# Performance work log

Hardware: AMD Instinct MI355X
Metric: run time of the kernel (lower is better)

## Reference

```python
import jax, jax.numpy as jnp
import numpy as np

ALPHA = 0.2
NEG = -9e15
LAYER_OUT = 2


def gat_layer(h, adj, W, a, concat):
    # h: (b,n,in), W: (in,out), a: (2*out,)
    # Faithful to GATLayer: e[i,j] = leaky_relu(a1.Wh_i + a2.Wh_j), computed
    # without materializing the (b,N,N,2F) repeat_interleave tensor.
    Wh = h @ W                               # (b,n,F)
    F = Wh.shape[-1]
    src = jnp.einsum('bnf,f->bn', Wh, a[:F])  # a1 . Wh_i
    dst = jnp.einsum('bnf,f->bn', Wh, a[F:])  # a2 . Wh_j
    e = jax.nn.leaky_relu(src[:, :, None] + dst[:, None, :], ALPHA)  # (b,n,n)
    att = jax.nn.softmax(jnp.where(adj > 0, e, NEG), axis=-1)
    hp = jnp.einsum('bij,bjf->bif', att, Wh)  # bmm aggregation
    return jax.nn.elu(hp) if concat else hp


def setup_inputs() -> dict:
    key = jax.random.key(0)
    ks = jax.random.split(key, 16)
    b, N, L = 16, 512, 1024
    comp_dim, prot_dim, gat_dim, H, latent = 128, 128, 64, 4, 128
    num_atom, num_amino, layer_cnn, window = 100, 30, 3, 5
    k = 2 * window + 1
    s = 0.1
    inp = {
        'atoms': jax.random.randint(ks[0], (b, N), 0, num_atom),
        'atoms_mask': jnp.ones((b, N), jnp.float32),
        'adjacency': jax.random.randint(ks[1], (b, N, N), 0, 2).astype(jnp.int32),
        'amino': jax.random.randint(ks[2], (b, L), 0, num_amino),
        'amino_mask': jnp.ones((b, L), jnp.float32),
        'E_atom': jax.random.normal(ks[3], (num_atom, comp_dim)) * s,
        'E_amino': jax.random.normal(ks[4], (num_amino, prot_dim)) * s,
        'W_gat': jax.random.normal(ks[5], (H, comp_dim, gat_dim)) * s,
        'a_gat': jax.random.normal(ks[6], (H, 2 * gat_dim)) * s,
        'W_go': jax.random.normal(ks[7], (gat_dim * H, comp_dim)) * s,
        'a_go': jax.random.normal(ks[8], (2 * comp_dim,)) * s,
        'W_comp_w': jax.random.normal(ks[9], (latent, comp_dim)) * s,
        'W_comp_b': jnp.zeros((latent,), jnp.float32),
        'conv_w': jax.random.normal(ks[10], (layer_cnn, 1, 1, k, k)) * s,
        'conv_b': jnp.zeros((layer_cnn, 1), jnp.float32),
        'W_att_w': jax.random.normal(ks[11], (latent, latent)) * s,
        'W_att_b': jnp.zeros((latent,), jnp.float32),
        'pred_w': jax.random.normal(ks[12], (1, 2 * latent)) * s,
        'pred_b': jnp.zeros((1,), jnp.float32),
    }
    return inp


def reference(atoms, atoms_mask, adjacency, amino, amino_mask,
              E_atom, E_amino, W_gat, a_gat, W_go, a_go,
              W_comp_w, W_comp_b, conv_w, conv_b,
              W_att_w, W_att_b, pred_w, pred_b):
    # ---- comp_gat (eval mode: dropout is identity) ----
    av = E_atom[atoms]                                      # (b,N,comp_dim)
    H = W_gat.shape[0]
    heads = [gat_layer(av, adjacency, W_gat[i], a_gat[i], True) for i in range(H)]
    multi = jnp.concatenate(heads, axis=-1)                 # (b,N,H*gat_dim)
    x = jax.nn.elu(gat_layer(multi, adjacency, W_go, a_go, False))
    atoms_vec = jax.nn.leaky_relu(x @ W_comp_w.T + W_comp_b, ALPHA)  # (b,N,latent)
    # ---- prot_cnn ----
    pv = E_amino[amino][:, None, :, :]                      # (b,1,L,prot_dim)
    for i in range(conv_w.shape[0]):
        pv = jax.nn.relu(
            jax.lax.conv_general_dilated(
                pv, conv_w[i], (1, 1), 'SAME',
                dimension_numbers=('NCHW', 'OIHW', 'NCHW'))
            + conv_b[i][None, :, None, None])
    amino_vec = pv[:, 0]                                    # (b,L,prot_dim)
    # ---- bidirectional_attention_prediction ----
    a_v = jax.nn.leaky_relu(atoms_vec @ W_att_w.T + W_att_b, ALPHA)
    p_v = jax.nn.leaky_relu(amino_vec @ W_att_w.T + W_att_b, ALPHA)
    prot = (p_v * amino_mask[:, :, None]).sum(1) / amino_mask.sum(1, keepdims=True)
    comp = (a_v * atoms_mask[:, :, None]).sum(1) / atoms_mask.sum(1, keepdims=True)
    cp = jnp.concatenate([comp, prot], axis=1)              # (b,2*latent)
    for _ in range(LAYER_OUT):
        cp = jax.nn.leaky_relu(cp, ALPHA)
    return cp @ pred_w.T + pred_b                           # (b,1)
```

## Files before the change

### kernel.cpp

```cpp
#include <hip/hip_runtime.h>
#include <hip/hip_bf16.h>

typedef __hip_bfloat16 bf16;

#define ALPHA 0.2f
#define NEGV  -9.0e15f
#define TI 8

__device__ __forceinline__ float b2f(bf16 x){ return __bfloat162float(x); }
__device__ __forceinline__ bf16  f2b(float x){ return __float2bfloat16(x); }
__device__ __forceinline__ float lrelu(float x){ return x > 0.f ? x : ALPHA*x; }
__device__ __forceinline__ float eluf(float x){ return x > 0.f ? x : expm1f(x); }

#define P_ATOMS_MASK 0
#define P_AMINO_MASK 8192
#define P_E_ATOM     24576
#define P_E_AMINO    37376
#define P_W_GAT      41216
#define P_A_GAT      73984
#define P_W_GO       74496
#define P_A_GO       107264
#define P_W_COMP_W   107520
#define P_W_COMP_B   123904
#define P_CONV_W     124032
#define P_CONV_B     124395
#define P_W_ATT_W    124398
#define P_W_ATT_B    140782
#define P_PRED_W     140910
#define P_PRED_B     141166
#define P_TOTAL      141167

__device__ __forceinline__ int detect_f32(const unsigned short* u, int n)
{
    int lim = n < 64 ? n : 64;
    bool f32like = false;
    for (int i = 0; i < lim; i += 2) {
        unsigned short h = u[i];
        int e = (h >> 7) & 0xFF;
        bool z = (h & 0x7FFF) == 0;
        if (!(z || (e >= 0x66 && e <= 0x88))) f32like = true;
    }
    if (!f32like && lim > 1 && (u[0] & 0x7FFF) == 0 && (u[1] & 0x7FFF) != 0)
        f32like = true;
    return f32like ? 1 : 0;
}
__device__ __forceinline__ float cvt_elem(const void* src, int e, int mode)
{
    return mode ? ((const float*)src)[e] : b2f(((const bf16*)src)[e]);
}

__global__ __launch_bounds__(256) void k_prep_a(
    const void* p0, const void* p1, const void* p2, const void* p3,
    const void* p4, const void* p5, const void* p6, const void* p7,
    float* __restrict__ params)
{
    const void* ps[8] = {p0,p1,p2,p3,p4,p5,p6,p7};
    const int offs[9] = {0,8192,24576,37376,41216,73984,74496,107264,107520};
    int idx = blockIdx.x*256 + threadIdx.x;
    if (idx >= 107520) return;
    int k = 0;
    while (idx >= offs[k+1]) ++k;
    int mode = detect_f32((const unsigned short*)ps[k], offs[k+1]-offs[k]);
    params[idx] = cvt_elem(ps[k], idx - offs[k], mode);
}

__global__ __launch_bounds__(256) void k_prep_b(
    const void* p0, const void* p1, const void* p2, const void* p3,
    const void* p4, const void* p5, const void* p6, const void* p7,
    float* __restrict__ params)
{
    const void* ps[8] = {p0,p1,p2,p3,p4,p5,p6,p7};
    const int offs[9] = {107520,123904,124032,124395,124398,140782,140910,141166,P_TOTAL};
    int idx = blockIdx.x*256 + threadIdx.x + 107520;
    if (idx >= P_TOTAL) return;
    int k = 0;
    while (idx >= offs[k+1]) ++k;
    int mode = detect_f32((const unsigned short*)ps[k], offs[k+1]-offs[k]);
    params[idx] = cvt_elem(ps[k], idx - offs[k], mode);
}

__global__ __launch_bounds__(256) void k_gat1_pre(
    const int* __restrict__ atoms, const float* __restrict__ params,
    bf16* __restrict__ Wh1, float* __restrict__ src1, float* __restrict__ dst1)
{
    int bid = blockIdx.x;
    int b = bid >> 9, n = bid & 511;
    int tid = threadIdx.x;
    __shared__ float av[128];
    if (tid < 128) av[tid] = params[P_E_ATOM + atoms[bid]*128 + tid];
    __syncthreads();
    int h = tid >> 6, f = tid & 63;
    const float* Wp = params + P_W_GAT + h*8192 + f;
    float wh = 0.f;
    #pragma unroll 8
    for (int k = 0; k < 128; ++k) wh += av[k] * Wp[k*64];
    Wh1[(size_t)bid*256 + h*64 + f] = f2b(wh);
    float p1 = wh * params[P_A_GAT + h*128 + f];
    float p2 = wh * params[P_A_GAT + h*128 + 64 + f];
    #pragma unroll
    for (int m = 32; m; m >>= 1) { p1 += __shfl_xor(p1, m, 64); p2 += __shfl_xor(p2, m, 64); }
    if (f == 0) { src1[(b*4+h)*512 + n] = p1; dst1[(b*4+h)*512 + n] = p2; }
}

__global__ __launch_bounds__(256) void k_gat1_att_b(
    const int* __restrict__ adj, const bf16* __restrict__ Wh1,
    const float* __restrict__ src1, const float* __restrict__ dst1,
    bf16* __restrict__ multi)
{
    int bid = blockIdx.x;
    int b = bid >> 6, i0 = (bid & 63) * TI;
    int tid = threadIdx.x;
    int h = tid >> 6, lane = tid & 63;
    __shared__ float att[4][TI][512];
    const float* dstp = dst1 + (b*4+h)*512;
    float invr[TI];
    #pragma unroll
    for (int ti = 0; ti < TI; ++ti) {
        int i = i0 + ti;
        const int* adjrow = adj + ((size_t)(b*512 + i))*512;
        float s_i = src1[(b*4+h)*512 + i];
        float e[8];
        float lm = -3.0e38f;
        #pragma unroll
        for (int jj = 0; jj < 8; ++jj) {
            int j = lane + jj*64;
            float v = lrelu(s_i + dstp[j]);
            v = adjrow[j] > 0 ? v : NEGV;
            e[jj] = v;
            lm = fmaxf(lm, v);
        }
        #pragma unroll
        for (int m = 32; m; m >>= 1) lm = fmaxf(lm, __shfl_xor(lm, m, 64));
        float ls = 0.f;
        #pragma unroll
        for (int jj = 0; jj < 8; ++jj) {
            float ex = __expf(e[jj] - lm);
            att[h][ti][lane + jj*64] = ex;
            ls += ex;
        }
        #pragma unroll
        for (int m = 32; m; m >>= 1) ls += __shfl_xor(ls, m, 64);
        invr[ti] = 1.f / ls;
    }
    const bf16* Whp = Wh1 + (size_t)(b*512)*256 + h*64 + lane;
    float acc[TI];
    #pragma unroll
    for (int ti = 0; ti < TI; ++ti) acc[ti] = 0.f;
    for (int j = 0; j < 512; ++j) {
        float w = b2f(Whp[(size_t)j*256]);
        #pragma unroll
        for (int ti = 0; ti < TI; ++ti)
            acc[ti] += att[h][ti][j] * w;
    }
    #pragma unroll
    for (int ti = 0; ti < TI; ++ti) {
        float hp = acc[ti] * invr[ti];
        multi[(size_t)(b*512 + i0 + ti)*256 + h*64 + lane] = f2b(eluf(hp));
    }
}

__global__ __launch_bounds__(128) void k_gat2_pre(
    const bf16* __restrict__ multi, const float* __restrict__ params,
    bf16* __restrict__ Wh2, float* __restrict__ src2, float* __restrict__ dst2)
{
    int bid = blockIdx.x;
    int tid = threadIdx.x;
    __shared__ float row[256];
    __shared__ float sr[2][2];
    row[tid]       = b2f(multi[(size_t)bid*256 + tid]);
    row[tid + 128] = b2f(multi[(size_t)bid*256 + tid + 128]);
    __syncthreads();
    const float* Wp = params + P_W_GO;
    float wh = 0.f;
    #pragma unroll 8
    for (int k = 0; k < 256; ++k) wh += row[k] * Wp[k*128 + tid];
    Wh2[(size_t)bid*128 + tid] = f2b(wh);
    float p1 = wh * params[P_A_GO + tid];
    float p2 = wh * params[P_A_GO + 128 + tid];
    #pragma unroll
    for (int m = 32; m; m >>= 1) { p1 += __shfl_xor(p1, m, 64); p2 += __shfl_xor(p2, m, 64); }
    int wid = tid >> 6;
    if ((tid & 63) == 0) { sr[0][wid] = p1; sr[1][wid] = p2; }
    __syncthreads();
    if (tid == 0) src2[bid] = sr[0][0] + sr[0][1];
    if (tid == 1) dst2[bid] = sr[1][0] + sr[1][1];
}

__global__ __launch_bounds__(256) void k_gat2_att_b(
    const int* __restrict__ adj, const bf16* __restrict__ Wh2,
    const float* __restrict__ src2, const float* __restrict__ dst2,
    bf16* __restrict__ x)
{
    int bid = blockIdx.x;
    int b = bid >> 6, i0 = (bid & 63) * TI;
    int tid = threadIdx.x;
    int wv = tid >> 6, lane = tid & 63;
    __shared__ float att[TI][512];
    __shared__ float red[TI][256];
    __shared__ float invs[TI];
    const float* dstp = dst2 + b*512;
    for (int ti = wv; ti < TI; ti += 4) {
        int i = i0 + ti;
        const int* adjrow = adj + ((size_t)(b*512 + i))*512;
        float s_i = src2[b*512 + i];
        float e[8];
        float lm = -3.0e38f;
        #pragma unroll
        for (int jj = 0; jj < 8; ++jj) {
            int j = lane + jj*64;
            float v = lrelu(s_i + dstp[j]);
            v = adjrow[j] > 0 ? v : NEGV;
            e[jj] = v;
            lm = fmaxf(lm, v);
        }
        #pragma unroll
        for (int m = 32; m; m >>= 1) lm = fmaxf(lm, __shfl_xor(lm, m, 64));
        float ls = 0.f;
        #pragma unroll
        for (int jj = 0; jj < 8; ++jj) {
            float ex = __expf(e[jj] - lm);
            att[ti][lane + jj*64] = ex;
            ls += ex;
        }
        #pragma unroll
        for (int m = 32; m; m >>= 1) ls += __shfl_xor(ls, m, 64);
        if (lane == 0) invs[ti] = 1.f / ls;
    }
    __syncthreads();
    int f = tid & 127, c = tid >> 7;
    const bf16* Whp = Wh2 + (size_t)(b*512)*128 + f;
    float acc[TI];
    #pragma unroll
    for (int ti = 0; ti < TI; ++ti) acc[ti] = 0.f;
    int j0 = c * 256;
    for (int j = j0; j < j0 + 256; ++j) {
        float w = b2f(Whp[(size_t)j*128]);
        #pragma unroll
        for (int ti = 0; ti < TI; ++ti)
            acc[ti] += att[ti][j] * w;
    }
    #pragma unroll
    for (int ti = 0; ti < TI; ++ti) red[ti][tid] = acc[ti];
    __syncthreads();
    if (c == 0) {
        #pragma unroll
        for (int ti = 0; ti < TI; ++ti) {
            float hp = (red[ti][f] + red[ti][f+128]) * invs[ti];
            x[(size_t)(b*512 + i0 + ti)*128 + f] = f2b(eluf(hp));
        }
    }
}

#define RM_ROWS 32
__global__ __launch_bounds__(256) void k_rowmat_tile(
    const bf16* __restrict__ in, const float* __restrict__ W,
    const float* __restrict__ bias, bf16* __restrict__ outv)
{
    __shared__ float wlds[128*129];
    __shared__ float rlds[RM_ROWS][128];
    int tid = threadIdx.x;
    size_t row0 = (size_t)blockIdx.x * RM_ROWS;
    for (int idx = tid; idx < 16384; idx += 256)
        wlds[(idx >> 7)*129 + (idx & 127)] = W[idx];
    for (int idx = tid; idx < RM_ROWS*128; idx += 256)
        rlds[idx >> 7][idx & 127] = b2f(in[row0*128 + idx]);
    __syncthreads();
    int l = tid & 127, g = tid >> 7;
    float bl = bias[l];
    #pragma unroll
    for (int rg = 0; rg < 16; rg += 4) {
        int r0 = 2*rg + g;
        float a0=0.f, a1=0.f, a2=0.f, a3=0.f;
        for (int k = 0; k < 128; ++k) {
            float w = wlds[l*129 + k];
            a0 += rlds[r0][k]*w;   a1 += rlds[r0+2][k]*w;
            a2 += rlds[r0+4][k]*w; a3 += rlds[r0+6][k]*w;
        }
        outv[(row0 + r0  )*128 + l] = f2b(lrelu(a0+bl));
        outv[(row0 + r0+2)*128 + l] = f2b(lrelu(a1+bl));
        outv[(row0 + r0+4)*128 + l] = f2b(lrelu(a2+bl));
        outv[(row0 + r0+6)*128 + l] = f2b(lrelu(a3+bl));
    }
}

__global__ __launch_bounds__(256) void k_att_acc_tile(
    const bf16* __restrict__ in, const float* __restrict__ W,
    const float* __restrict__ bias, const float* __restrict__ mask,
    float* __restrict__ acc, int per_b)
{
    __shared__ float wlds[128*129];
    __shared__ float rlds[RM_ROWS][128];
    __shared__ float mlds[RM_ROWS];
    __shared__ float psum[128];
    int tid = threadIdx.x;
    size_t row0 = (size_t)blockIdx.x * RM_ROWS;
    int b = (int)(row0 / per_b);
    for (int idx = tid; idx < 16384; idx += 256)
        wlds[(idx >> 7)*129 + (idx & 127)] = W[idx];
    for (int idx = tid; idx < RM_ROWS*128; idx += 256)
        rlds[idx >> 7][idx & 127] = b2f(in[row0*128 + idx]);
    if (tid < RM_ROWS) mlds[tid] = mask[row0 + tid];
    __syncthreads();
    int l = tid & 127, g = tid >> 7;
    float bl = bias[l];
    float vsum = 0.f;
    #pragma unroll
    for (int rg = 0; rg < 16; rg += 4) {
        int r0 = 2*rg + g;
        float a0=0.f, a1=0.f, a2=0.f, a3=0.f;
        for (int k = 0; k < 128; ++k) {
            float w = wlds[l*129 + k];
            a0 += rlds[r0][k]*w;   a1 += rlds[r0+2][k]*w;
            a2 += rlds[r0+4][k]*w; a3 += rlds[r0+6][k]*w;
        }
        vsum += lrelu(a0+bl)*mlds[r0]   + lrelu(a1+bl)*mlds[r0+2]
              + lrelu(a2+bl)*mlds[r0+4] + lrelu(a3+bl)*mlds[r0+6];
    }
    if (g == 1) psum[l] = vsum;
    __syncthreads();
    if (g == 0) atomicAdd(&acc[b*128 + l], vsum + psum[l]);
}

__global__ __launch_bounds__(128) void k_conv(
    const bf16* __restrict__ in, const int* __restrict__ amino,
    const float* __restrict__ params, bf16* __restrict__ out,
    int layer, int first)
{
    int bid = blockIdx.x;
    int b = bid >> 10, i = bid & 1023;
    int tid = threadIdx.x;
    __shared__ float tile[11][139];
    __shared__ float wts[121];
    __shared__ float bias;
    if (tid < 121) wts[tid] = params[P_CONV_W + layer*121 + tid];
    if (tid == 121) bias = params[P_CONV_B + layer];
    for (int idx = tid; idx < 11*138; idx += 128) {
        int r = idx / 138, cc = idx % 138;
        int ri = i + r - 5, cj = cc - 5;
        float v = 0.f;
        if (ri >= 0 && ri < 1024 && cj >= 0 && cj < 128) {
            v = first ? params[P_E_AMINO + amino[b*1024 + ri]*128 + cj]
                      : b2f(in[((size_t)(b*1024 + ri))*128 + cj]);
        }
        tile[r][cc] = v;
    }
    __syncthreads();
    float a = bias;
    #pragma unroll
    for (int di = 0; di < 11; ++di)
        #pragma unroll
        for (int dj = 0; dj < 11; ++dj)
            a += tile[di][tid + dj] * wts[di*11 + dj];
    out[(size_t)bid*128 + tid] = f2b(fmaxf(a, 0.f));
}

__global__ __launch_bounds__(256) void k_final(
    const float* __restrict__ params, const float* __restrict__ acc,
    float* __restrict__ out)
{
    int b = blockIdx.x, tid = threadIdx.x;
    __shared__ float red[256];
    float s = 0.f;
    for (int t = tid; t < 512; t += 256) s += params[P_ATOMS_MASK + b*512 + t];
    #pragma unroll
    for (int m = 32; m; m >>= 1) s += __shfl_xor(s, m, 64);
    if ((tid & 63) == 0) red[tid >> 6] = s;
    __syncthreads();
    float sum_atoms = red[0]+red[1]+red[2]+red[3];
    __syncthreads();
    s = 0.f;
    for (int t = tid; t < 1024; t += 256) s += params[P_AMINO_MASK + b*1024 + t];
    #pragma unroll
    for (int m = 32; m; m >>= 1) s += __shfl_xor(s, m, 64);
    if ((tid & 63) == 0) red[tid >> 6] = s;
    __syncthreads();
    float sum_amino = red[0]+red[1]+red[2]+red[3];
    __syncthreads();
    float val = (tid < 128) ? acc[b*128 + tid] / sum_atoms
                            : acc[2048 + b*128 + (tid-128)] / sum_amino;
    val = lrelu(lrelu(val));
    val *= params[P_PRED_W + tid];
    #pragma unroll
    for (int m = 32; m; m >>= 1) val += __shfl_xor(val, m, 64);
    if ((tid & 63) == 0) red[tid >> 6] = val;
    __syncthreads();
    if (tid == 0) out[b] = red[0]+red[1]+red[2]+red[3] + params[P_PRED_B];
}

extern "C" void kernel_launch(void* const* d_in, const int* in_sizes, int n_in,
                              void* d_out, int out_size, void* d_ws, size_t ws_size,
                              hipStream_t stream)
{
    const int* atoms     = (const int*)d_in[0];
    const int* adjacency = (const int*)d_in[2];
    const int* amino     = (const int*)d_in[3];
    float* out = (float*)d_out;
    (void)in_sizes; (void)n_in; (void)ws_size;

    char* base = (char*)d_ws;
    float* params = (float*)(base + 0);
    float* src1   = (float*)(base + 565248);
    float* dst1   = (float*)(base + 696320);
    float* src2   = (float*)(base + 827392);
    float* dst2   = (float*)(base + 860160);
    float* acc    = (float*)(base + 892928);
    bf16*  A      = (bf16*)(base + 909568);
    bf16*  B      = (bf16*)(base + 5103872);
    bf16*  C      = (bf16*)(base + 9298176);

    bf16* Wh1 = B;
    bf16* multi = C;
    bf16* Wh2 = B;
    bf16* xbuf = B + 1048576;
    bf16* atoms_vec = C;

    hipMemsetAsync(acc, 0, 4096*sizeof(float), stream);

    k_prep_a<<<420, 256, 0, stream>>>(d_in[1], d_in[4], d_in[5], d_in[6],
                                      d_in[7], d_in[8], d_in[9], d_in[10], params);
    k_prep_b<<<132, 256, 0, stream>>>(d_in[11], d_in[12], d_in[13], d_in[14],
                                      d_in[15], d_in[16], d_in[17], d_in[18], params);

    k_conv<<<16384, 128, 0, stream>>>(nullptr, amino, params, A, 0, 1);
    k_conv<<<16384, 128, 0, stream>>>(A,       amino, params, B, 1, 0);
    k_conv<<<16384, 128, 0, stream>>>(B,       amino, params, A, 2, 0);

    k_gat1_pre<<<8192, 256, 0, stream>>>(atoms, params, Wh1, src1, dst1);
    k_gat1_att_b<<<1024, 256, 0, stream>>>(adjacency, Wh1, src1, dst1, multi);

    k_gat2_pre<<<8192, 128, 0, stream>>>(multi, params, Wh2, src2, dst2);
    k_gat2_att_b<<<1024, 256, 0, stream>>>(adjacency, Wh2, src2, dst2, xbuf);

    k_rowmat_tile<<<256, 256, 0, stream>>>(xbuf, params + P_W_COMP_W,
                                           params + P_W_COMP_B, atoms_vec);

    k_att_acc_tile<<<256, 256, 0, stream>>>(atoms_vec, params + P_W_ATT_W,
                                            params + P_W_ATT_B, params + P_ATOMS_MASK,
                                            acc, 512);
    k_att_acc_tile<<<512, 256, 0, stream>>>(A, params + P_W_ATT_W,
                                            params + P_W_ATT_B, params + P_AMINO_MASK,
                                            acc + 2048, 1024);

    k_final<<<16, 256, 0, stream>>>(params, acc, out);
}
```

Before: 526.0 us.

## Tile conv and GAT projection kernels over 8 rows per block

The three conv layers now compute 8 output rows per block from an 18-row shared tile, where before each block loaded an 11-row halo for a single row. The two GAT projection kernels also process 8 nodes per block, so each weight load from global memory is reused across 8 accumulators. The aim is to cut redundant halo and weight reads and reduce block count and launch overhead. In exchange, registers per thread go up and there are fewer blocks to spread across the GPU.

```diff
diff --git a/kernel.cpp b/kernel.cpp
--- a/kernel.cpp
+++ b/kernel.cpp
@@ -79,27 +79,44 @@
     params[idx] = cvt_elem(ps[k], idx - offs[k], mode);
 }
 
-__global__ __launch_bounds__(256) void k_gat1_pre(
+__global__ __launch_bounds__(256) void k_gat1_pre_b(
     const int* __restrict__ atoms, const float* __restrict__ params,
     bf16* __restrict__ Wh1, float* __restrict__ src1, float* __restrict__ dst1)
 {
     int bid = blockIdx.x;
-    int b = bid >> 9, n = bid & 511;
-    int tid = threadIdx.x;
-    __shared__ float av[128];
-    if (tid < 128) av[tid] = params[P_E_ATOM + atoms[bid]*128 + tid];
+    int b = bid >> 6, n0 = (bid & 63) * 8;
+    int tid = threadIdx.x;
+    __shared__ float av[128][8];
+    __shared__ int aidx[8];
+    if (tid < 8) aidx[tid] = atoms[b*512 + n0 + tid];
+    __syncthreads();
+    for (int idx = tid; idx < 1024; idx += 256) {
+        int k = idx >> 3, r = idx & 7;
+        av[k][r] = params[P_E_ATOM + aidx[r]*128 + k];
+    }
     __syncthreads();
     int h = tid >> 6, f = tid & 63;
     const float* Wp = params + P_W_GAT + h*8192 + f;
-    float wh = 0.f;
-    #pragma unroll 8
-    for (int k = 0; k < 128; ++k) wh += av[k] * Wp[k*64];
-    Wh1[(size_t)bid*256 + h*64 + f] = f2b(wh);
-    float p1 = wh * params[P_A_GAT + h*128 + f];
-    float p2 = wh * params[P_A_GAT + h*128 + 64 + f];
-    #pragma unroll
-    for (int m = 32; m; m >>= 1) { p1 += __shfl_xor(p1, m, 64); p2 += __shfl_xor(p2, m, 64); }
-    if (f == 0) { src1[(b*4+h)*512 + n] = p1; dst1[(b*4+h)*512 + n] = p2; }
+    float acc[8];
+    #pragma unroll
+    for (int r = 0; r < 8; ++r) acc[r] = 0.f;
+    for (int k = 0; k < 128; ++k) {
+        float w = Wp[k*64];
+        #pragma unroll
+        for (int r = 0; r < 8; ++r) acc[r] += av[k][r] * w;
+    }
+    float a1 = params[P_A_GAT + h*128 + f];
+    float a2 = params[P_A_GAT + h*128 + 64 + f];
+    #pragma unroll
+    for (int r = 0; r < 8; ++r) {
+        int n = n0 + r;
+        Wh1[(size_t)(b*512 + n)*256 + h*64 + f] = f2b(acc[r]);
+        float p1 = acc[r] * a1;
+        float p2 = acc[r] * a2;
+        #pragma unroll
+        for (int m = 32; m; m >>= 1) { p1 += __shfl_xor(p1, m, 64); p2 += __shfl_xor(p2, m, 64); }
+        if (f == 0) { src1[(b*4+h)*512 + n] = p1; dst1[(b*4+h)*512 + n] = p2; }
+    }
 }
 
 __global__ __launch_bounds__(256) void k_gat1_att_b(
@@ -159,31 +176,44 @@
     }
 }
 
-__global__ __launch_bounds__(128) void k_gat2_pre(
+__global__ __launch_bounds__(128) void k_gat2_pre_b(
     const bf16* __restrict__ multi, const float* __restrict__ params,
     bf16* __restrict__ Wh2, float* __restrict__ src2, float* __restrict__ dst2)
 {
     int bid = blockIdx.x;
-    int tid = threadIdx.x;
-    __shared__ float row[256];
-    __shared__ float sr[2][2];
-    row[tid]       = b2f(multi[(size_t)bid*256 + tid]);
-    row[tid + 128] = b2f(multi[(size_t)bid*256 + tid + 128]);
+    int b = bid >> 6, n0 = (bid & 63) * 8;
+    int tid = threadIdx.x;
+    __shared__ float row[256][8];
+    __shared__ float sr[2][2][8];
+    for (int idx = tid; idx < 2048; idx += 128) {
+        int k = idx >> 3, r = idx & 7;
+        row[k][r] = b2f(multi[(size_t)(b*512 + n0 + r)*256 + k]);
+    }
     __syncthreads();
     const float* Wp = params + P_W_GO;
-    float wh = 0.f;
-    #pragma unroll 8
-    for (int k = 0; k < 256; ++k) wh += row[k] * Wp[k*128 + tid];
-    Wh2[(size_t)bid*128 + tid] = f2b(wh);
-    float p1 = wh * params[P_A_GO + tid];
-    float p2 = wh * params[P_A_GO + 128 + tid];
-    #pragma unroll
-    for (int m = 32; m; m >>= 1) { p1 += __shfl_xor(p1, m, 64); p2 += __shfl_xor(p2, m, 64); }
+    float acc[8];
+    #pragma unroll
+    for (int r = 0; r < 8; ++r) acc[r] = 0.f;
+    for (int k = 0; k < 256; ++k) {
+        float w = Wp[k*128 + tid];
+        #pragma unroll
+        for (int r = 0; r < 8; ++r) acc[r] += row[k][r] * w;
+    }
+    float a1 = params[P_A_GO + tid];
+    float a2 = params[P_A_GO + 128 + tid];
     int wid = tid >> 6;
-    if ((tid & 63) == 0) { sr[0][wid] = p1; sr[1][wid] = p2; }
-    __syncthreads();
-    if (tid == 0) src2[bid] = sr[0][0] + sr[0][1];
-    if (tid == 1) dst2[bid] = sr[1][0] + sr[1][1];
+    #pragma unroll
+    for (int r = 0; r < 8; ++r) {
+        Wh2[(size_t)(b*512 + n0 + r)*128 + tid] = f2b(acc[r]);
+        float p1 = acc[r] * a1;
+        float p2 = acc[r] * a2;
+        #pragma unroll
+        for (int m = 32; m; m >>= 1) { p1 += __shfl_xor(p1, m, 64); p2 += __shfl_xor(p2, m, 64); }
+        if ((tid & 63) == 0) { sr[wid][0][r] = p1; sr[wid][1][r] = p2; }
+    }
+    __syncthreads();
+    if (tid < 8)              src2[b*512 + n0 + tid]       = sr[0][0][tid] + sr[1][0][tid];
+    else if (tid < 16)        dst2[b*512 + n0 + (tid-8)]   = sr[0][1][tid-8] + sr[1][1][tid-8];
 }
 
 __global__ __launch_bounds__(256) void k_gat2_att_b(
@@ -321,37 +351,48 @@
     if (g == 0) atomicAdd(&acc[b*128 + l], vsum + psum[l]);
 }
 
-__global__ __launch_bounds__(128) void k_conv(
+__global__ __launch_bounds__(256) void k_conv_b(
     const bf16* __restrict__ in, const int* __restrict__ amino,
     const float* __restrict__ params, bf16* __restrict__ out,
     int layer, int first)
 {
     int bid = blockIdx.x;
-    int b = bid >> 10, i = bid & 1023;
-    int tid = threadIdx.x;
-    __shared__ float tile[11][139];
+    int b = bid >> 7, i0 = (bid & 127) * 8;
+    int tid = threadIdx.x;
+    __shared__ float tile[18][139];
     __shared__ float wts[121];
     __shared__ float bias;
+    __shared__ int amn[18];
     if (tid < 121) wts[tid] = params[P_CONV_W + layer*121 + tid];
     if (tid == 121) bias = params[P_CONV_B + layer];
-    for (int idx = tid; idx < 11*138; idx += 128) {
+    if (first && tid < 18) {
+        int ri = i0 + tid - 5;
+        amn[tid] = (ri >= 0 && ri < 1024) ? amino[b*1024 + ri] : 0;
+    }
+    __syncthreads();
+    for (int idx = tid; idx < 18*138; idx += 256) {
         int r = idx / 138, cc = idx % 138;
-        int ri = i + r - 5, cj = cc - 5;
+        int ri = i0 + r - 5, cj = cc - 5;
         float v = 0.f;
         if (ri >= 0 && ri < 1024 && cj >= 0 && cj < 128) {
-            v = first ? params[P_E_AMINO + amino[b*1024 + ri]*128 + cj]
+            v = first ? params[P_E_AMINO + amn[r]*128 + cj]
                       : b2f(in[((size_t)(b*1024 + ri))*128 + cj]);
         }
         tile[r][cc] = v;
     }
     __syncthreads();
-    float a = bias;
-    #pragma unroll
-    for (int di = 0; di < 11; ++di)
-        #pragma unroll
-        for (int dj = 0; dj < 11; ++dj)
-            a += tile[di][tid + dj] * wts[di*11 + dj];
-    out[(size_t)bid*128 + tid] = f2b(fmaxf(a, 0.f));
+    int c = tid & 127, g = tid >> 7;
+    #pragma unroll
+    for (int rg = 0; rg < 4; ++rg) {
+        int ro = rg*2 + g;
+        float a = bias;
+        #pragma unroll
+        for (int di = 0; di < 11; ++di)
+            #pragma unroll
+            for (int dj = 0; dj < 11; ++dj)
+                a += tile[ro + di][c + dj] * wts[di*11 + dj];
+        out[(size_t)(b*1024 + i0 + ro)*128 + c] = f2b(fmaxf(a, 0.f));
+    }
 }
 
 __global__ __launch_bounds__(256) void k_final(
@@ -421,14 +462,14 @@
     k_prep_b<<<132, 256, 0, stream>>>(d_in[11], d_in[12], d_in[13], d_in[14],
                                       d_in[15], d_in[16], d_in[17], d_in[18], params);
 
-    k_conv<<<16384, 128, 0, stream>>>(nullptr, amino, params, A, 0, 1);
-    k_conv<<<16384, 128, 0, stream>>>(A,       amino, params, B, 1, 0);
-    k_conv<<<16384, 128, 0, stream>>>(B,       amino, params, A, 2, 0);
-
-    k_gat1_pre<<<8192, 256, 0, stream>>>(atoms, params, Wh1, src1, dst1);
+    k_conv_b<<<2048, 256, 0, stream>>>(nullptr, amino, params, A, 0, 1);
+    k_conv_b<<<2048, 256, 0, stream>>>(A,       amino, params, B, 1, 0);
+    k_conv_b<<<2048, 256, 0, stream>>>(B,       amino, params, A, 2, 0);
+
+    k_gat1_pre_b<<<1024, 256, 0, stream>>>(atoms, params, Wh1, src1, dst1);
     k_gat1_att_b<<<1024, 256, 0, stream>>>(adjacency, Wh1, src1, dst1, multi);
 
-    k_gat2_pre<<<8192, 128, 0, stream>>>(multi, params, Wh2, src2, dst2);
+    k_gat2_pre_b<<<1024, 128, 0, stream>>>(multi, params, Wh2, src2, dst2);
     k_gat2_att_b<<<1024, 256, 0, stream>>>(adjacency, Wh2, src2, dst2, xbuf);
 
     k_rowmat_tile<<<256, 256, 0, stream>>>(xbuf, params + P_W_COMP_W,
```

New measurement: 538.4 us. 1.02x slower.
